# Kernel optimization log

Measured on AMD Instinct MI355X. Metric: run time of the kernel, lower is better.

The kernel has to match this reference:

```python
import jax, jax.numpy as jnp
import numpy as np

SEQ, D, H, P, FINAL = 2048, 1024, 16, 64, 1024


def setup_inputs() -> dict:
    key = jax.random.key(0)
    k_x, k_q, k_k, k_v, k_w = jax.random.split(key, 5)
    return {
        "x": jax.random.normal(k_x, (SEQ, D), dtype=jnp.float32),
        "Qw": jax.random.uniform(k_q, (H, D, P), dtype=jnp.float32),
        "Kw": jax.random.uniform(k_k, (H, D, P), dtype=jnp.float32),
        "Vw": jax.random.uniform(k_v, (H, D, P), dtype=jnp.float32),
        "W_fin": jax.random.normal(k_w, (H * P, FINAL), dtype=jnp.float32) * (1.0 / np.sqrt(H * P)),
        "b_fin": jnp.zeros((FINAL,), dtype=jnp.float32),
    }


def reference(x, Qw, Kw, Vw, W_fin, b_fin):
    # x: [S, D]; Qw/Kw/Vw: [H, D, P]
    Q = jnp.einsum("sd,hdp->hsp", x, Qw)  # [H, S, P]
    K = jnp.einsum("sd,hdp->hsp", x, Kw)
    V = jnp.einsum("sd,hdp->hsp", x, Vw)
    p_dim = K.shape[-1]
    # sigmoid attention: no row-wise normalization, scale by P (not sqrt(P))
    score = jax.nn.sigmoid(jnp.einsum("hsp,htp->hst", Q, K) / p_dim)  # [H, S, S]
    attn = jnp.einsum("hst,htp->hsp", score, V)  # [H, S, P]
    # faithful raw reshape (torch .reshape(seq, -1) on contiguous [H, S, P])
    concat = attn.reshape(x.shape[0], -1)  # [S, H*P]
    return concat @ W_fin + b_fin  # [S, FINAL]
```

## Files before the change

### kernel.cpp

```cpp
#include <hip/hip_runtime.h>
#include <hip/hip_bf16.h>

#define SEQL 2048
#define DMODEL 1024
#define NH 16
#define HEADP 64
#define FINALD 1024

using bf16x8 = __attribute__((ext_vector_type(8))) short;
using f32x4  = __attribute__((ext_vector_type(4))) float;
using s16x4  = __attribute__((ext_vector_type(4))) short;

__device__ __forceinline__ f32x4 mfma16(bf16x8 a, bf16x8 b, f32x4 c) {
  return __builtin_amdgcn_mfma_f32_16x16x32_bf16(a, b, c, 0, 0, 0);
}

__device__ __forceinline__ unsigned short f2bf(float f) {
  return __builtin_bit_cast(unsigned short, __float2bfloat16(f));
}

__device__ __forceinline__ void gload16(const void* g, void* l) {
  __builtin_amdgcn_global_load_lds(
      (const __attribute__((address_space(1))) void*)g,
      (__attribute__((address_space(3))) void*)l, 16, 0, 0);
}

__global__ void k_f32_to_bf16(const float* __restrict__ src,
                              unsigned short* __restrict__ dst, int n4) {
  int i = blockIdx.x * blockDim.x + threadIdx.x;
  if (i >= n4) return;
  float4 v = reinterpret_cast<const float4*>(src)[i];
  ushort4 o;
  o.x = f2bf(v.x); o.y = f2bf(v.y); o.z = f2bf(v.z); o.w = f2bf(v.w);
  reinterpret_cast<ushort4*>(dst)[i] = o;
}

__global__ __launch_bounds__(256) void k_prep(
    const float* __restrict__ Qw, const float* __restrict__ Kw,
    const float* __restrict__ Vw, const float* __restrict__ Wf,
    unsigned short* __restrict__ Wt, unsigned short* __restrict__ WfT) {
  __shared__ float tile[64][65];
  int z = blockIdx.z;
  const float* src; unsigned short* dst;
  int C, tr = blockIdx.x * 64, tc;
  if (z < 3) {
    const float* s3 = (z == 0) ? Qw : (z == 1) ? Kw : Vw;
    src = s3 + (long)blockIdx.y * 65536;
    dst = Wt + (long)z * 1048576 + (long)blockIdx.y * 65536;
    C = 64; tc = 0;
  } else {
    src = Wf; dst = WfT; C = 1024; tc = blockIdx.y * 64;
  }
  const int R = 1024;
  int t = threadIdx.x;
  int r0 = t >> 4, c4 = (t & 15) * 4;
#pragma unroll
  for (int i = 0; i < 4; ++i) {
    int r = i * 16 + r0;
    float4 v = *reinterpret_cast<const float4*>(src + (long)(tr + r) * C + tc + c4);
    tile[r][c4 + 0] = v.x; tile[r][c4 + 1] = v.y;
    tile[r][c4 + 2] = v.z; tile[r][c4 + 3] = v.w;
  }
  __syncthreads();
  int r4 = (t & 15) * 4, cc0 = t >> 4;
#pragma unroll
  for (int i = 0; i < 4; ++i) {
    int c = i * 16 + cc0;
    ushort4 o;
    o.x = f2bf(tile[r4 + 0][c]); o.y = f2bf(tile[r4 + 1][c]);
    o.z = f2bf(tile[r4 + 2][c]); o.w = f2bf(tile[r4 + 3][c]);
    *reinterpret_cast<ushort4*>(dst + (long)(tc + c) * R + tr + r4) = o;
  }
}

template <int EPI>
__global__ __launch_bounds__(256) void k_gemm(
    const unsigned short* __restrict__ A,
    const unsigned short* __restrict__ Bt,
    int K,
    unsigned short* __restrict__ Qb,
    unsigned short* __restrict__ Kb,
    unsigned short* __restrict__ Vtb,
    const float* __restrict__ bias,
    float* __restrict__ outf) {
  __shared__ char lds[24576];
  int m0 = blockIdx.x * 128, n0 = blockIdx.y * 64;
  int t = threadIdx.x;
  int l = t & 63, w = t >> 6;
  int r = l & 15, g = l >> 4;
  int wr = w >> 1, wc = w & 1;

  const unsigned short* Arow = A + (long)m0 * K;
  const unsigned short* Brow = Bt + (long)n0 * K;
  int rr = l >> 2, c8 = (l & 3) * 8;

  auto stage = [&](int buf, int k0) {
    char* base = lds + buf * 12288;
    char* dA = base + w * 2048;
    char* dB = base + 8192 + w * 1024;
    gload16(Arow + (long)(w * 32 + rr) * K + k0 + c8, dA);
    gload16(Arow + (long)(w * 32 + 16 + rr) * K + k0 + c8, dA + 1024);
    gload16(Brow + (long)(w * 16 + rr) * K + k0 + c8, dB);
  };

  f32x4 acc[4][2] = {};
  int cur = 0, NK = K / 32;
  stage(0, 0);
  __syncthreads();
  for (int kt = 0; kt < NK; ++kt) {
    if (kt + 1 < NK) stage(cur ^ 1, (kt + 1) * 32);
    const char* As = lds + cur * 12288;
    const char* Bs = As + 8192;
    bf16x8 af[4], bb[2];
#pragma unroll
    for (int i = 0; i < 4; ++i)
      af[i] = *reinterpret_cast<const bf16x8*>(As + (wr * 64 + i * 16 + r) * 64 + g * 16);
#pragma unroll
    for (int i = 0; i < 2; ++i)
      bb[i] = *reinterpret_cast<const bf16x8*>(Bs + (wc * 32 + i * 16 + r) * 64 + g * 16);
#pragma unroll
    for (int mi = 0; mi < 4; ++mi)
#pragma unroll
      for (int ni = 0; ni < 2; ++ni)
        acc[mi][ni] = mfma16(af[mi], bb[ni], acc[mi][ni]);
    __syncthreads();
    cur ^= 1;
  }

  if constexpr (EPI == 0) {
    int which = n0 >> 10;
    int hb = (n0 & 1023) >> 6;
    if (which < 2) {
      unsigned short* dst = (which == 0 ? Qb : Kb) + (long)hb * SEQL * HEADP;
#pragma unroll
      for (int mi = 0; mi < 4; ++mi) {
        int s0 = m0 + wr * 64 + mi * 16 + g * 4;
#pragma unroll
        for (int ni = 0; ni < 2; ++ni) {
          int p = wc * 32 + ni * 16 + r;
#pragma unroll
          for (int v = 0; v < 4; ++v)
            dst[(long)(s0 + v) * HEADP + p] = f2bf(acc[mi][ni][v]);
        }
      }
    } else {
      unsigned short* dst = Vtb + (long)hb * HEADP * SEQL;
#pragma unroll
      for (int mi = 0; mi < 4; ++mi) {
        int s0 = m0 + wr * 64 + mi * 16 + g * 4;
#pragma unroll
        for (int ni = 0; ni < 2; ++ni) {
          int p = wc * 32 + ni * 16 + r;
          ushort4 pk;
          pk.x = f2bf(acc[mi][ni][0]); pk.y = f2bf(acc[mi][ni][1]);
          pk.z = f2bf(acc[mi][ni][2]); pk.w = f2bf(acc[mi][ni][3]);
          *reinterpret_cast<ushort4*>(dst + (long)p * SEQL + s0) = pk;
        }
      }
    }
  } else {
#pragma unroll
    for (int ni = 0; ni < 2; ++ni) {
      int c = n0 + wc * 32 + ni * 16 + r;
      float bv = bias[c];
#pragma unroll
      for (int mi = 0; mi < 4; ++mi) {
        int s0 = m0 + wr * 64 + mi * 16 + g * 4;
#pragma unroll
        for (int v = 0; v < 4; ++v)
          outf[(long)(s0 + v) * FINALD + c] = acc[mi][ni][v] + bv;
      }
    }
  }
}

__global__ __launch_bounds__(256) void k_attn(
    const unsigned short* __restrict__ Qb,
    const unsigned short* __restrict__ Kb,
    const unsigned short* __restrict__ Vtb,
    unsigned short* __restrict__ Ab) {
  __shared__ char lds[40960];
  int b = blockIdx.x;
  int xcd = b & 7, j = b >> 3;
  int h = (xcd << 1) | (j & 1);
  int sblk = j >> 1;
  int lane = threadIdx.x & 63, wave = threadIdx.x >> 6;
  int r = lane & 15, g = lane >> 4;
  int q0 = sblk * 64 + wave * 16;
  const unsigned short* Qh = Qb + ((long)h * SEQL + q0) * HEADP;
  const unsigned short* Kh = Kb + (long)h * SEQL * HEADP;
  const unsigned short* Vh = Vtb + (long)h * HEADP * SEQL;

  bf16x8 qf0 = *reinterpret_cast<const bf16x8*>(Qh + (long)r * HEADP + g * 8);
  bf16x8 qf1 = *reinterpret_cast<const bf16x8*>(Qh + (long)r * HEADP + 32 + g * 8);

  f32x4 z4 = {0.f, 0.f, 0.f, 0.f};
  f32x4 oacc[4] = {z4, z4, z4, z4};
  char* slab = lds + 32768 + wave * 2048;
  int swz = (r & 7) << 4;
  const float CLN = -0.02254211001389005f;

  int sub = lane >> 3, chunk = lane & 7;
  auto stage = [&](int buf, int t0) {
    char* kb = lds + buf * 16384 + wave * 2048;
    char* vb = kb + 8192;
#pragma unroll
    for (int jj = 0; jj < 2; ++jj) {
      int row = wave * 16 + jj * 8 + sub;
      int sw = (chunk ^ (row & 7)) * 8;
      gload16(Kh + (long)(t0 + row) * HEADP + sw, kb + jj * 1024);
      gload16(Vh + (long)row * SEQL + t0 + sw, vb + jj * 1024);
    }
  };

  int cur = 0;
  stage(0, 0);
  __syncthreads();
  for (int t0 = 0; t0 < SEQL; t0 += 64) {
    if (t0 + 64 < SEQL) stage(cur ^ 1, t0 + 64);

    const char* kb = lds + cur * 16384;
    const char* vb = kb + 8192;
    f32x4 s[4] = {z4, z4, z4, z4};
#pragma unroll
    for (int tb = 0; tb < 4; ++tb) {
      const char* krow = kb + (tb * 16 + r) * 128;
      bf16x8 k0 = *reinterpret_cast<const bf16x8*>(krow + ((g ^ (r & 7)) * 16));
      bf16x8 k1 = *reinterpret_cast<const bf16x8*>(krow + (((4 + g) ^ (r & 7)) * 16));
      s[tb] = mfma16(k0, qf0, s[tb]);
      s[tb] = mfma16(k1, qf1, s[tb]);
    }
#pragma unroll
    for (int tb = 0; tb < 4; ++tb) {
      s16x4 pk;
#pragma unroll
      for (int v = 0; v < 4; ++v) {
        float e = __builtin_amdgcn_exp2f(s[tb][v] * CLN);
        pk[v] = (short)f2bf(__builtin_amdgcn_rcpf(1.0f + e));
      }
      *reinterpret_cast<s16x4*>(slab + r * 128 + ((tb * 32 + g * 8) ^ swz)) = pk;
    }
    bf16x8 pa0 = *reinterpret_cast<const bf16x8*>(slab + r * 128 + ((g * 16) ^ swz));
    bf16x8 pa1 = *reinterpret_cast<const bf16x8*>(slab + r * 128 + ((64 + g * 16) ^ swz));
#pragma unroll
    for (int nb = 0; nb < 4; ++nb) {
      const char* vrow = vb + (nb * 16 + r) * 128;
      bf16x8 v0 = *reinterpret_cast<const bf16x8*>(vrow + ((g ^ (r & 7)) * 16));
      bf16x8 v1 = *reinterpret_cast<const bf16x8*>(vrow + (((4 + g) ^ (r & 7)) * 16));
      oacc[nb] = mfma16(pa0, v0, oacc[nb]);
      oacc[nb] = mfma16(pa1, v1, oacc[nb]);
    }
    __syncthreads();
    cur ^= 1;
  }
  unsigned short* Oh = Ab + ((long)h * SEQL + q0) * HEADP;
#pragma unroll
  for (int nb = 0; nb < 4; ++nb)
#pragma unroll
    for (int v = 0; v < 4; ++v)
      Oh[(g * 4 + v) * HEADP + nb * 16 + r] = f2bf(oacc[nb][v]);
}

extern "C" void kernel_launch(void* const* d_in, const int* in_sizes, int n_in,
                              void* d_out, int out_size, void* d_ws, size_t ws_size,
                              hipStream_t stream) {
  const float* x  = (const float*)d_in[0];
  const float* Qw = (const float*)d_in[1];
  const float* Kw = (const float*)d_in[2];
  const float* Vw = (const float*)d_in[3];
  const float* Wf = (const float*)d_in[4];
  const float* bf = (const float*)d_in[5];
  float* out = (float*)d_out;

  unsigned short* ws  = (unsigned short*)d_ws;
  unsigned short* xb  = ws;
  unsigned short* Wt  = ws + 2097152;
  unsigned short* WfT = ws + 5242880;
  unsigned short* Qb  = ws + 6291456;
  unsigned short* Kb  = ws + 8388608;
  unsigned short* Vtb = ws + 10485760;
  unsigned short* Ab  = ws + 12582912;

  k_f32_to_bf16<<<2048, 256, 0, stream>>>(x, xb, 524288);
  k_prep<<<dim3(16, 16, 4), 256, 0, stream>>>(Qw, Kw, Vw, Wf, Wt, WfT);
  k_gemm<0><<<dim3(16, 48), 256, 0, stream>>>(xb, Wt, DMODEL, Qb, Kb, Vtb, nullptr, nullptr);
  k_attn<<<512, 256, 0, stream>>>(Qb, Kb, Vtb, Ab);
  k_gemm<1><<<dim3(16, 16), 256, 0, stream>>>(Ab, WfT, DMODEL, nullptr, nullptr, nullptr, bf, out);
}
```

Measured before the change: 87.20 us.

## Fuse x conversion into prep kernel, double GEMM K-tile, prioritize MFMA in attention

The separate f32-to-bf16 conversion of x is folded into the prep kernel as a fifth z-slice, removing one kernel launch. The GEMM K-step per iteration grows from 32 to 64, which doubles shared memory per block and halves the number of barriers and pipeline stages. In the attention loop, s_setprio raises wave priority around the MFMA sections so matrix work can interleave better with the sigmoid math in other waves. The larger LDS footprint may lower occupancy in the GEMMs.

```diff
diff --git a/kernel.cpp b/kernel.cpp
--- a/kernel.cpp
+++ b/kernel.cpp
@@ -25,22 +25,27 @@
       (__attribute__((address_space(3))) void*)l, 16, 0, 0);
 }
 
-__global__ void k_f32_to_bf16(const float* __restrict__ src,
-                              unsigned short* __restrict__ dst, int n4) {
-  int i = blockIdx.x * blockDim.x + threadIdx.x;
-  if (i >= n4) return;
-  float4 v = reinterpret_cast<const float4*>(src)[i];
-  ushort4 o;
-  o.x = f2bf(v.x); o.y = f2bf(v.y); o.z = f2bf(v.z); o.w = f2bf(v.w);
-  reinterpret_cast<ushort4*>(dst)[i] = o;
-}
-
 __global__ __launch_bounds__(256) void k_prep(
     const float* __restrict__ Qw, const float* __restrict__ Kw,
     const float* __restrict__ Vw, const float* __restrict__ Wf,
-    unsigned short* __restrict__ Wt, unsigned short* __restrict__ WfT) {
+    const float* __restrict__ x,
+    unsigned short* __restrict__ Wt, unsigned short* __restrict__ WfT,
+    unsigned short* __restrict__ xb) {
   __shared__ float tile[64][65];
   int z = blockIdx.z;
+  int t = threadIdx.x;
+  if (z == 4) {
+    long i0 = ((long)blockIdx.y * 16 + blockIdx.x) * 2048 + t;
+#pragma unroll
+    for (int k = 0; k < 8; ++k) {
+      long i = i0 + k * 256;
+      float4 v = reinterpret_cast<const float4*>(x)[i];
+      ushort4 o;
+      o.x = f2bf(v.x); o.y = f2bf(v.y); o.z = f2bf(v.z); o.w = f2bf(v.w);
+      reinterpret_cast<ushort4*>(xb)[i] = o;
+    }
+    return;
+  }
   const float* src; unsigned short* dst;
   int C, tr = blockIdx.x * 64, tc;
   if (z < 3) {
@@ -52,7 +57,6 @@
     src = Wf; dst = WfT; C = 1024; tc = blockIdx.y * 64;
   }
   const int R = 1024;
-  int t = threadIdx.x;
   int r0 = t >> 4, c4 = (t & 15) * 4;
 #pragma unroll
   for (int i = 0; i < 4; ++i) {
@@ -83,7 +87,7 @@
     unsigned short* __restrict__ Vtb,
     const float* __restrict__ bias,
     float* __restrict__ outf) {
-  __shared__ char lds[24576];
+  __shared__ char lds[49152];
   int m0 = blockIdx.x * 128, n0 = blockIdx.y * 64;
   int t = threadIdx.x;
   int l = t & 63, w = t >> 6;
@@ -95,34 +99,42 @@
   int rr = l >> 2, c8 = (l & 3) * 8;
 
   auto stage = [&](int buf, int k0) {
-    char* base = lds + buf * 12288;
-    char* dA = base + w * 2048;
-    char* dB = base + 8192 + w * 1024;
-    gload16(Arow + (long)(w * 32 + rr) * K + k0 + c8, dA);
-    gload16(Arow + (long)(w * 32 + 16 + rr) * K + k0 + c8, dA + 1024);
-    gload16(Brow + (long)(w * 16 + rr) * K + k0 + c8, dB);
+    char* base = lds + buf * 24576;
+#pragma unroll
+    for (int kk = 0; kk < 2; ++kk) {
+      char* dA = base + kk * 8192 + w * 2048;
+      char* dB = base + 16384 + kk * 4096 + w * 1024;
+      int kc = k0 + kk * 32 + c8;
+      gload16(Arow + (long)(w * 32 + rr) * K + kc, dA);
+      gload16(Arow + (long)(w * 32 + 16 + rr) * K + kc, dA + 1024);
+      gload16(Brow + (long)(w * 16 + rr) * K + kc, dB);
+    }
   };
 
   f32x4 acc[4][2] = {};
-  int cur = 0, NK = K / 32;
+  int cur = 0, NK = K / 64;
   stage(0, 0);
   __syncthreads();
   for (int kt = 0; kt < NK; ++kt) {
-    if (kt + 1 < NK) stage(cur ^ 1, (kt + 1) * 32);
-    const char* As = lds + cur * 12288;
-    const char* Bs = As + 8192;
-    bf16x8 af[4], bb[2];
-#pragma unroll
-    for (int i = 0; i < 4; ++i)
-      af[i] = *reinterpret_cast<const bf16x8*>(As + (wr * 64 + i * 16 + r) * 64 + g * 16);
-#pragma unroll
-    for (int i = 0; i < 2; ++i)
-      bb[i] = *reinterpret_cast<const bf16x8*>(Bs + (wc * 32 + i * 16 + r) * 64 + g * 16);
-#pragma unroll
-    for (int mi = 0; mi < 4; ++mi)
-#pragma unroll
-      for (int ni = 0; ni < 2; ++ni)
-        acc[mi][ni] = mfma16(af[mi], bb[ni], acc[mi][ni]);
+    if (kt + 1 < NK) stage(cur ^ 1, (kt + 1) * 64);
+    const char* base = lds + cur * 24576;
+#pragma unroll
+    for (int kk = 0; kk < 2; ++kk) {
+      const char* As = base + kk * 8192;
+      const char* Bs = base + 16384 + kk * 4096;
+      bf16x8 af[4], bb[2];
+#pragma unroll
+      for (int i = 0; i < 4; ++i)
+        af[i] = *reinterpret_cast<const bf16x8*>(As + (wr * 64 + i * 16 + r) * 64 + g * 16);
+#pragma unroll
+      for (int i = 0; i < 2; ++i)
+        bb[i] = *reinterpret_cast<const bf16x8*>(Bs + (wc * 32 + i * 16 + r) * 64 + g * 16);
+#pragma unroll
+      for (int mi = 0; mi < 4; ++mi)
+#pragma unroll
+        for (int ni = 0; ni < 2; ++ni)
+          acc[mi][ni] = mfma16(af[mi], bb[ni], acc[mi][ni]);
+    }
     __syncthreads();
     cur ^= 1;
   }
@@ -222,6 +234,7 @@
     const char* kb = lds + cur * 16384;
     const char* vb = kb + 8192;
     f32x4 s[4] = {z4, z4, z4, z4};
+    __builtin_amdgcn_s_setprio(1);
 #pragma unroll
     for (int tb = 0; tb < 4; ++tb) {
       const char* krow = kb + (tb * 16 + r) * 128;
@@ -230,6 +243,7 @@
       s[tb] = mfma16(k0, qf0, s[tb]);
       s[tb] = mfma16(k1, qf1, s[tb]);
     }
+    __builtin_amdgcn_s_setprio(0);
 #pragma unroll
     for (int tb = 0; tb < 4; ++tb) {
       s16x4 pk;
@@ -242,6 +256,7 @@
     }
     bf16x8 pa0 = *reinterpret_cast<const bf16x8*>(slab + r * 128 + ((g * 16) ^ swz));
     bf16x8 pa1 = *reinterpret_cast<const bf16x8*>(slab + r * 128 + ((64 + g * 16) ^ swz));
+    __builtin_amdgcn_s_setprio(1);
 #pragma unroll
     for (int nb = 0; nb < 4; ++nb) {
       const char* vrow = vb + (nb * 16 + r) * 128;
@@ -250,6 +265,7 @@
       oacc[nb] = mfma16(pa0, v0, oacc[nb]);
       oacc[nb] = mfma16(pa1, v1, oacc[nb]);
     }
+    __builtin_amdgcn_s_setprio(0);
     __syncthreads();
     cur ^= 1;
   }
@@ -281,8 +297,7 @@
   unsigned short* Vtb = ws + 10485760;
   unsigned short* Ab  = ws + 12582912;
 
-  k_f32_to_bf16<<<2048, 256, 0, stream>>>(x, xb, 524288);
-  k_prep<<<dim3(16, 16, 4), 256, 0, stream>>>(Qw, Kw, Vw, Wf, Wt, WfT);
+  k_prep<<<dim3(16, 16, 5), 256, 0, stream>>>(Qw, Kw, Vw, Wf, x, Wt, WfT, xb);
   k_gemm<0><<<dim3(16, 48), 256, 0, stream>>>(xb, Wt, DMODEL, Qb, Kb, Vtb, nullptr, nullptr);
   k_attn<<<512, 256, 0, stream>>>(Qb, Kb, Vtb, Ab);
   k_gemm<1><<<dim3(16, 16), 256, 0, stream>>>(Ab, WfT, DMODEL, nullptr, nullptr, nullptr, bf, out);
```

Result: faster. 80.73 us (-7.4%).
